# Kernel tuning notes

Hardware: AMD Instinct MI355X
Metric: run time of the kernel (lower is better)

Reference implementation:

```python
import jax, jax.numpy as jnp
import numpy as np

B, NR, IC, NC, OC = 64, 16384, 16, 10, 16
NUM_ITERS = 3


def setup_inputs() -> dict:
    key = jax.random.key(0)
    k1, k2, k3, k4 = jax.random.split(key, 4)
    x = jax.random.normal(k1, (B, NR, IC), dtype=jnp.float32)
    W = jax.random.normal(k2, (IC, NC, OC, NR), dtype=jnp.float32)
    fc_w = jax.random.normal(k3, (1, NC * OC), dtype=jnp.float32)
    fc_b = jax.random.normal(k4, (1,), dtype=jnp.float32)
    return {"x": x, "W": W, "fc_w": fc_w, "fc_b": fc_b}


def _squash(s):
    # Original squash is applied to tensors with trailing dim of size 1,
    # so the norm reduction is elementwise: s^2 * s / ((1+s^2) * sqrt(s^2))
    sq = s * s
    return sq * s / ((1.0 + sq) * jnp.sqrt(sq))


def reference(x, W, fc_w, fc_b):
    batch = x.shape[0]
    in_ch, nc, oc, nr = W.shape
    # u_hat[b,i,c,o] = sum_r W[i,c,o,r] * x[b,r,i]  (x is identical across capsules)
    u_hat = jnp.einsum('icor,bri->bico', W, x)  # [B, in_ch, nc, oc]
    b_ij = jnp.zeros((in_ch, nc), dtype=x.dtype)
    v_j = None
    for it in range(NUM_ITERS):
        c_ij = jax.nn.softmax(b_ij, axis=0)              # softmax over in_channels
        s_j = jnp.einsum('ic,bico->bco', c_ij, u_hat)    # [B, nc, oc]
        v_j = _squash(s_j)
        if it < NUM_ITERS - 1:
            # agreement a[b,i,c] = sum_o u_hat[b,i,c,o] * v[b,c,o]; mean over batch
            a_ij = jnp.einsum('bico,bco->ic', u_hat, v_j) / batch
            b_ij = b_ij + a_ij
    pred = jax.nn.sigmoid(v_j.reshape(batch, -1) @ fc_w.T + fc_b)[:, 0]  # [B]
    return pred, v_j[..., None]  # v_j returned as [B, nc, oc, 1] like torch
```

## Files before the change

### kernel.cpp

```cpp
#include <hip/hip_runtime.h>

typedef unsigned int uint;
typedef unsigned short ushort;
typedef __attribute__((ext_vector_type(8))) short bf16x8;
typedef __attribute__((ext_vector_type(4))) float floatx4;
typedef __attribute__((ext_vector_type(4))) uint uint4v;

#define B_   64
#define NR_  16384
#define IC_  16
#define NC_  10
#define OC_  16
#define NCO  160
#define KC_  32
#define KT_  32

__device__ __forceinline__ float bf2f(ushort h) {
    return __uint_as_float(((uint)h) << 16);
}
__device__ __forceinline__ ushort f2bf(float f) {
    uint u = __float_as_uint(f);
    u += 0x7fffu + ((u >> 16) & 1u);
    return (ushort)(u >> 16);
}
__device__ __forceinline__ void splitbf(float f, ushort& h, ushort& l) {
    h = f2bf(f);
    l = f2bf(f - bf2f(h));
}
__device__ __forceinline__ float squashf(float s) {
    return s * fabsf(s) / (1.0f + s * s);
}

__global__ __launch_bounds__(256) void k_xT(const float* __restrict__ xf,
                                            ushort* __restrict__ xTh,
                                            ushort* __restrict__ xTl)
{
    const int chunk = blockIdx.x, b = blockIdx.y, t = threadIdx.x;
    const int r0 = chunk * 1024;
#pragma unroll
    for (int j = 0; j < 4; ++j) {
        int r = r0 + t + 256 * j;
        const float* row = xf + ((size_t)b * NR_ + r) * IC_;
        float vals[16];
        *(float4*)&vals[0]  = *(const float4*)row;
        *(float4*)&vals[4]  = *(const float4*)(row + 4);
        *(float4*)&vals[8]  = *(const float4*)(row + 8);
        *(float4*)&vals[12] = *(const float4*)(row + 12);
#pragma unroll
        for (int i = 0; i < 16; ++i) {
            ushort h, l;
            splitbf(vals[i], h, l);
            size_t idx = ((size_t)(i * B_ + b)) * NR_ + r;
            xTh[idx] = h;
            xTl[idx] = l;
        }
    }
}

__global__ __launch_bounds__(512) void k_uhat(const float* __restrict__ xf,
                                              const float* __restrict__ wf,
                                              const ushort* __restrict__ xTh,
                                              const ushort* __restrict__ xTl,
                                              int has_xt,
                                              float* __restrict__ uh)
{
    const int i    = blockIdx.x;
    const int kc   = blockIdx.y;
    const int tid  = threadIdx.x;
    const int lane = tid & 63;
    const int w    = tid >> 6;
    const int quad = lane >> 4;
    const int m16  = lane & 15;
    const int bt   = w & 3;
    const int cg   = w >> 2;

    __shared__ ushort Xh[64 * 40], Xl[64 * 40];
    __shared__ ushort Wh[160 * 40], Wl[160 * 40];

    floatx4 acc[5];
#pragma unroll
    for (int t = 0; t < 5; ++t) acc[t] = (floatx4){0.f, 0.f, 0.f, 0.f};

    const int r0 = kc * (NR_ / KC_);

    for (int st = 0; st < (NR_ / KC_) / KT_; ++st) {
        const int rb = r0 + st * KT_;
        __syncthreads();
        if (has_xt) {
            int t8 = tid & 255, bb = t8 >> 2, part = t8 & 3;
            size_t src = (size_t)(i * B_ + bb) * NR_ + rb + part * 8;
            if (tid < 256)
                *(uint4v*)&Xh[bb * 40 + part * 8] = *(const uint4v*)&xTh[src];
            else
                *(uint4v*)&Xl[bb * 40 + part * 8] = *(const uint4v*)&xTl[src];
        } else {
#pragma unroll
            for (int s = 0; s < 4; ++s) {
                int n = tid + 512 * s;
                int bb = n >> 5, k = n & 31;
                float v = xf[(size_t)bb * (NR_ * IC_) + (size_t)(rb + k) * IC_ + i];
                ushort h, l;
                splitbf(v, h, l);
                Xh[bb * 40 + k] = h;
                Xl[bb * 40 + k] = l;
            }
        }
        for (int j = tid; j < 640; j += 512) {
            int row = j >> 2, seg = j & 3;
            const float* wp = wf + (size_t)(i * NCO + row) * NR_ + rb + seg * 8;
            float4 f0 = *(const float4*)wp;
            float4 f1 = *(const float4*)(wp + 4);
            float v[8] = {f0.x, f0.y, f0.z, f0.w, f1.x, f1.y, f1.z, f1.w};
            ushort hh[8], ll[8];
#pragma unroll
            for (int q = 0; q < 8; ++q) splitbf(v[q], hh[q], ll[q]);
            uint4v ph, pl;
#pragma unroll
            for (int q = 0; q < 4; ++q) {
                ph[q] = (uint)hh[2 * q] | ((uint)hh[2 * q + 1] << 16);
                pl[q] = (uint)ll[2 * q] | ((uint)ll[2 * q + 1] << 16);
            }
            *(uint4v*)&Wh[row * 40 + seg * 8] = ph;
            *(uint4v*)&Wl[row * 40 + seg * 8] = pl;
        }
        __syncthreads();
        bf16x8 afh = *(const bf16x8*)&Xh[(bt * 16 + m16) * 40 + quad * 8];
        bf16x8 afl = *(const bf16x8*)&Xl[(bt * 16 + m16) * 40 + quad * 8];
#pragma unroll
        for (int t = 0; t < 5; ++t) {
            int corow = (cg * 5 + t) * 16 + m16;
            bf16x8 bh = *(const bf16x8*)&Wh[corow * 40 + quad * 8];
            bf16x8 bl = *(const bf16x8*)&Wl[corow * 40 + quad * 8];
            acc[t] = __builtin_amdgcn_mfma_f32_16x16x32_bf16(afh, bh, acc[t], 0, 0, 0);
            acc[t] = __builtin_amdgcn_mfma_f32_16x16x32_bf16(afl, bh, acc[t], 0, 0, 0);
            acc[t] = __builtin_amdgcn_mfma_f32_16x16x32_bf16(afh, bl, acc[t], 0, 0, 0);
        }
    }
#pragma unroll
    for (int t = 0; t < 5; ++t) {
        int co = (cg * 5 + t) * 16 + m16;
#pragma unroll
        for (int r = 0; r < 4; ++r) {
            int b = bt * 16 + quad * 4 + r;
            atomicAdd(&uh[(b * IC_ + i) * NCO + co], acc[t][r]);
        }
    }
}

__global__ __launch_bounds__(256) void k_route1(const float* __restrict__ uh,
                                                float* __restrict__ a1)
{
    const int b = blockIdx.x, tid = threadIdx.x;
    __shared__ float vL[NCO];
    const float* ub = uh + b * IC_ * NCO;
    if (tid < NCO) {
        float s = 0.f;
#pragma unroll
        for (int i = 0; i < IC_; ++i) s += ub[i * NCO + tid];
        vL[tid] = squashf(s * (1.0f / 16.0f));
    }
    __syncthreads();
    if (tid < NCO) {
        int i = tid / NC_, c = tid - i * NC_;
        float sum = 0.f;
#pragma unroll
        for (int o = 0; o < OC_; ++o)
            sum += ub[i * NCO + c * OC_ + o] * vL[c * OC_ + o];
        atomicAdd(&a1[i * NC_ + c], sum * (1.0f / 64.0f));
    }
}

__global__ __launch_bounds__(256) void k_route2(const float* __restrict__ uh,
                                                const float* __restrict__ a1,
                                                float* __restrict__ a2)
{
    const int b = blockIdx.x, tid = threadIdx.x;
    __shared__ float aL[NCO];
    __shared__ float vL[NCO];
    if (tid < NCO) aL[tid] = a1[tid];
    __syncthreads();
    const float* ub = uh + b * IC_ * NCO;
    if (tid < NCO) {
        int c = tid >> 4;
        float m = -1e30f;
        for (int i = 0; i < IC_; ++i) m = fmaxf(m, aL[i * NC_ + c]);
        float Z = 0.f;
        for (int i = 0; i < IC_; ++i) Z += expf(aL[i * NC_ + c] - m);
        float s = 0.f;
        for (int i = 0; i < IC_; ++i)
            s += (expf(aL[i * NC_ + c] - m) / Z) * ub[i * NCO + tid];
        vL[tid] = squashf(s);
    }
    __syncthreads();
    if (tid < NCO) {
        int i = tid / NC_, c = tid - i * NC_;
        float sum = 0.f;
#pragma unroll
        for (int o = 0; o < OC_; ++o)
            sum += ub[i * NCO + c * OC_ + o] * vL[c * OC_ + o];
        atomicAdd(&a2[i * NC_ + c], sum * (1.0f / 64.0f));
    }
}

__global__ __launch_bounds__(256) void k_route3(const float* __restrict__ uh,
                                                const float* __restrict__ a1,
                                                const float* __restrict__ a2,
                                                const float* __restrict__ fcw,
                                                const float* __restrict__ fcb,
                                                float* __restrict__ out)
{
    const int b = blockIdx.x, tid = threadIdx.x;
    __shared__ float bL[NCO];
    __shared__ float pL[NCO];
    if (tid < NCO) bL[tid] = a1[tid] + a2[tid];
    __syncthreads();
    const float* ub = uh + b * IC_ * NCO;
    if (tid < NCO) {
        int c = tid >> 4;
        float m = -1e30f;
        for (int i = 0; i < IC_; ++i) m = fmaxf(m, bL[i * NC_ + c]);
        float Z = 0.f;
        for (int i = 0; i < IC_; ++i) Z += expf(bL[i * NC_ + c] - m);
        float s = 0.f;
        for (int i = 0; i < IC_; ++i)
            s += (expf(bL[i * NC_ + c] - m) / Z) * ub[i * NCO + tid];
        float v = squashf(s);
        out[64 + b * NCO + tid] = v;
        pL[tid] = v * fcw[tid];
    }
    __syncthreads();
    if (tid == 0) {
        float accv = fcb[0];
        for (int j = 0; j < NCO; ++j) accv += pL[j];
        out[b] = 1.0f / (1.0f + expf(-accv));
    }
}

extern "C" void kernel_launch(void* const* d_in, const int* in_sizes, int n_in,
                              void* d_out, int out_size, void* d_ws, size_t ws_size,
                              hipStream_t stream)
{
    const float* x   = (const float*)d_in[0];
    const float* W   = (const float*)d_in[1];
    const float* fcw = (const float*)d_in[2];
    const float* fcb = (const float*)d_in[3];
    float* out = (float*)d_out;

    float* uh = (float*)d_ws;
    float* a1 = uh + B_ * IC_ * NCO;
    float* a2 = a1 + NCO;
    const size_t xt_off   = 1u << 20;
    const size_t xt_bytes = (size_t)IC_ * B_ * NR_ * 2;
    ushort* xTh = (ushort*)((char*)d_ws + xt_off);
    ushort* xTl = (ushort*)((char*)d_ws + xt_off + xt_bytes);
    const int has_xt = (ws_size >= xt_off + 2 * xt_bytes) ? 1 : 0;

    hipMemsetAsync(d_ws, 0, (size_t)(B_ * IC_ * NCO + 2 * NCO) * sizeof(float), stream);
    if (has_xt)
        k_xT<<<dim3(16, 64), 256, 0, stream>>>(x, xTh, xTl);
    k_uhat<<<dim3(IC_, KC_), 512, 0, stream>>>(x, W, xTh, xTl, has_xt, uh);
    k_route1<<<B_, 256, 0, stream>>>(uh, a1);
    k_route2<<<B_, 256, 0, stream>>>(uh, a1, a2);
    k_route3<<<B_, 256, 0, stream>>>(uh, a1, a2, fcw, fcb, out);
}
```

Measured before the change: 321.8 us.

## Double-buffer W tiles in uhat GEMM and fuse routing into one kernel

```diff
diff --git a/kernel.cpp b/kernel.cpp
--- a/kernel.cpp
+++ b/kernel.cpp
@@ -4,7 +4,6 @@
 typedef unsigned short ushort;
 typedef __attribute__((ext_vector_type(8))) short bf16x8;
 typedef __attribute__((ext_vector_type(4))) float floatx4;
-typedef __attribute__((ext_vector_type(4))) uint uint4v;
 
 #define B_   64
 #define NR_  16384
@@ -14,6 +13,7 @@
 #define NCO  160
 #define KC_  32
 #define KT_  32
+#define NSTEP 16
 
 __device__ __forceinline__ float bf2f(ushort h) {
     return __uint_as_float(((uint)h) << 16);
@@ -33,9 +33,15 @@
 
 __global__ __launch_bounds__(256) void k_xT(const float* __restrict__ xf,
                                             ushort* __restrict__ xTh,
-                                            ushort* __restrict__ xTl)
+                                            ushort* __restrict__ xTl,
+                                            float* __restrict__ uh)
 {
     const int chunk = blockIdx.x, b = blockIdx.y, t = threadIdx.x;
+    if (chunk == 0) {
+        float4 z = {0.f, 0.f, 0.f, 0.f};
+        float4* dst = (float4*)(uh + (size_t)b * (IC_ * NCO));
+        for (int n = t; n < 640; n += 256) dst[n] = z;
+    }
     const int r0 = chunk * 1024;
 #pragma unroll
     for (int j = 0; j < 4; ++j) {
@@ -57,12 +63,80 @@
     }
 }
 
-__global__ __launch_bounds__(512) void k_uhat(const float* __restrict__ xf,
-                                              const float* __restrict__ wf,
-                                              const ushort* __restrict__ xTh,
-                                              const ushort* __restrict__ xTl,
-                                              int has_xt,
-                                              float* __restrict__ uh)
+__device__ __forceinline__ void loadW5(const float* __restrict__ wbase_st,
+                                       int tid, float2* r)
+{
+#pragma unroll
+    for (int s = 0; s < 5; ++s) {
+        int idx2 = tid + 512 * s;
+        int row  = idx2 >> 4;
+        int e    = idx2 & 15;
+        r[s] = *(const float2*)(wbase_st + (size_t)row * NR_ + 2 * e);
+    }
+}
+
+__device__ __forceinline__ void storeW5(const float2* r, int tid,
+                                        ushort* __restrict__ WhB,
+                                        ushort* __restrict__ WlB)
+{
+#pragma unroll
+    for (int s = 0; s < 5; ++s) {
+        int idx2 = tid + 512 * s;
+        int row  = idx2 >> 4;
+        int e    = idx2 & 15;
+        ushort h0, l0, h1, l1;
+        splitbf(r[s].x, h0, l0);
+        splitbf(r[s].y, h1, l1);
+        *(uint*)&WhB[row * 40 + 2 * e] = (uint)h0 | ((uint)h1 << 16);
+        *(uint*)&WlB[row * 40 + 2 * e] = (uint)l0 | ((uint)l1 << 16);
+    }
+}
+
+__device__ __forceinline__ void loadX(const ushort* __restrict__ xTh,
+                                      const ushort* __restrict__ xTl,
+                                      size_t xrow, int st, int has_xt,
+                                      const float* __restrict__ xf,
+                                      int b, int i, int r0, int quad,
+                                      bf16x8& h, bf16x8& l)
+{
+    if (has_xt) {
+        size_t o = xrow + (size_t)st * KT_;
+        h = *(const bf16x8*)&xTh[o];
+        l = *(const bf16x8*)&xTl[o];
+    } else {
+#pragma unroll
+        for (int q = 0; q < 8; ++q) {
+            float v = xf[((size_t)b * NR_ + r0 + st * KT_ + quad * 8 + q) * IC_ + i];
+            ushort hh, ll;
+            splitbf(v, hh, ll);
+            h[q] = (short)hh;
+            l[q] = (short)ll;
+        }
+    }
+}
+
+__device__ __forceinline__ void mfma5(const ushort* __restrict__ WhB,
+                                      const ushort* __restrict__ WlB,
+                                      bf16x8 ah, bf16x8 al,
+                                      floatx4* acc, int cg, int m16, int quad)
+{
+#pragma unroll
+    for (int t5 = 0; t5 < 5; ++t5) {
+        int corow = (cg * 5 + t5) * 16 + m16;
+        bf16x8 bh = *(const bf16x8*)&WhB[corow * 40 + quad * 8];
+        bf16x8 bl = *(const bf16x8*)&WlB[corow * 40 + quad * 8];
+        acc[t5] = __builtin_amdgcn_mfma_f32_16x16x32_bf16(ah, bh, acc[t5], 0, 0, 0);
+        acc[t5] = __builtin_amdgcn_mfma_f32_16x16x32_bf16(al, bh, acc[t5], 0, 0, 0);
+        acc[t5] = __builtin_amdgcn_mfma_f32_16x16x32_bf16(ah, bl, acc[t5], 0, 0, 0);
+    }
+}
+
+__global__ __launch_bounds__(512, 4) void k_uhat(const float* __restrict__ xf,
+                                                 const float* __restrict__ wf,
+                                                 const ushort* __restrict__ xTh,
+                                                 const ushort* __restrict__ xTl,
+                                                 int has_xt,
+                                                 float* __restrict__ uh)
 {
     const int i    = blockIdx.x;
     const int kc   = blockIdx.y;
@@ -74,165 +148,173 @@
     const int bt   = w & 3;
     const int cg   = w >> 2;
 
-    __shared__ ushort Xh[64 * 40], Xl[64 * 40];
-    __shared__ ushort Wh[160 * 40], Wl[160 * 40];
+    __shared__ ushort Wh[2][160 * 40];
+    __shared__ ushort Wl[2][160 * 40];
 
     floatx4 acc[5];
 #pragma unroll
     for (int t = 0; t < 5; ++t) acc[t] = (floatx4){0.f, 0.f, 0.f, 0.f};
 
     const int r0 = kc * (NR_ / KC_);
-
-    for (int st = 0; st < (NR_ / KC_) / KT_; ++st) {
-        const int rb = r0 + st * KT_;
+    const float* wbase = wf + (size_t)i * NCO * NR_ + r0;
+    const int xb = bt * 16 + m16;
+    const size_t xrow = (size_t)(i * B_ + xb) * NR_ + r0 + quad * 8;
+
+    float2 wA[5], wB[5];
+    bf16x8 xhA, xlA, xhB, xlB;
+
+    loadW5(wbase, tid, wA);
+    loadX(xTh, xTl, xrow, 0, has_xt, xf, xb, i, r0, quad, xhA, xlA);
+    storeW5(wA, tid, Wh[0], Wl[0]);
+    loadW5(wbase + 1 * KT_, tid, wB);
+    __syncthreads();
+
+    for (int st = 0; st < NSTEP; st += 2) {
+        loadX(xTh, xTl, xrow, st + 1, has_xt, xf, xb, i, r0, quad, xhB, xlB);
+        storeW5(wB, tid, Wh[1], Wl[1]);
+        if (st + 2 < NSTEP) loadW5(wbase + (size_t)(st + 2) * KT_, tid, wA);
+        mfma5(Wh[0], Wl[0], xhA, xlA, acc, cg, m16, quad);
         __syncthreads();
-        if (has_xt) {
-            int t8 = tid & 255, bb = t8 >> 2, part = t8 & 3;
-            size_t src = (size_t)(i * B_ + bb) * NR_ + rb + part * 8;
-            if (tid < 256)
-                *(uint4v*)&Xh[bb * 40 + part * 8] = *(const uint4v*)&xTh[src];
-            else
-                *(uint4v*)&Xl[bb * 40 + part * 8] = *(const uint4v*)&xTl[src];
-        } else {
-#pragma unroll
-            for (int s = 0; s < 4; ++s) {
-                int n = tid + 512 * s;
-                int bb = n >> 5, k = n & 31;
-                float v = xf[(size_t)bb * (NR_ * IC_) + (size_t)(rb + k) * IC_ + i];
-                ushort h, l;
-                splitbf(v, h, l);
-                Xh[bb * 40 + k] = h;
-                Xl[bb * 40 + k] = l;
-            }
-        }
-        for (int j = tid; j < 640; j += 512) {
-            int row = j >> 2, seg = j & 3;
-            const float* wp = wf + (size_t)(i * NCO + row) * NR_ + rb + seg * 8;
-            float4 f0 = *(const float4*)wp;
-            float4 f1 = *(const float4*)(wp + 4);
-            float v[8] = {f0.x, f0.y, f0.z, f0.w, f1.x, f1.y, f1.z, f1.w};
-            ushort hh[8], ll[8];
-#pragma unroll
-            for (int q = 0; q < 8; ++q) splitbf(v[q], hh[q], ll[q]);
-            uint4v ph, pl;
-#pragma unroll
-            for (int q = 0; q < 4; ++q) {
-                ph[q] = (uint)hh[2 * q] | ((uint)hh[2 * q + 1] << 16);
-                pl[q] = (uint)ll[2 * q] | ((uint)ll[2 * q + 1] << 16);
-            }
-            *(uint4v*)&Wh[row * 40 + seg * 8] = ph;
-            *(uint4v*)&Wl[row * 40 + seg * 8] = pl;
-        }
+
+        if (st + 2 < NSTEP) {
+            loadX(xTh, xTl, xrow, st + 2, has_xt, xf, xb, i, r0, quad, xhA, xlA);
+            storeW5(wA, tid, Wh[0], Wl[0]);
+        }
+        if (st + 3 < NSTEP) loadW5(wbase + (size_t)(st + 3) * KT_, tid, wB);
+        mfma5(Wh[1], Wl[1], xhB, xlB, acc, cg, m16, quad);
         __syncthreads();
-        bf16x8 afh = *(const bf16x8*)&Xh[(bt * 16 + m16) * 40 + quad * 8];
-        bf16x8 afl = *(const bf16x8*)&Xl[(bt * 16 + m16) * 40 + quad * 8];
-#pragma unroll
-        for (int t = 0; t < 5; ++t) {
-            int corow = (cg * 5 + t) * 16 + m16;
-            bf16x8 bh = *(const bf16x8*)&Wh[corow * 40 + quad * 8];
-            bf16x8 bl = *(const bf16x8*)&Wl[corow * 40 + quad * 8];
-            acc[t] = __builtin_amdgcn_mfma_f32_16x16x32_bf16(afh, bh, acc[t], 0, 0, 0);
-            acc[t] = __builtin_amdgcn_mfma_f32_16x16x32_bf16(afl, bh, acc[t], 0, 0, 0);
-            acc[t] = __builtin_amdgcn_mfma_f32_16x16x32_bf16(afh, bl, acc[t], 0, 0, 0);
-        }
-    }
-#pragma unroll
-    for (int t = 0; t < 5; ++t) {
-        int co = (cg * 5 + t) * 16 + m16;
+    }
+
+#pragma unroll
+    for (int t5 = 0; t5 < 5; ++t5) {
+        int co = (cg * 5 + t5) * 16 + m16;
 #pragma unroll
         for (int r = 0; r < 4; ++r) {
             int b = bt * 16 + quad * 4 + r;
-            atomicAdd(&uh[(b * IC_ + i) * NCO + co], acc[t][r]);
-        }
-    }
-}
-
-__global__ __launch_bounds__(256) void k_route1(const float* __restrict__ uh,
-                                                float* __restrict__ a1)
-{
-    const int b = blockIdx.x, tid = threadIdx.x;
-    __shared__ float vL[NCO];
-    const float* ub = uh + b * IC_ * NCO;
-    if (tid < NCO) {
+            atomicAdd(&uh[(b * IC_ + i) * NCO + co], acc[t5][r]);
+        }
+    }
+}
+
+__global__ __launch_bounds__(256) void k_route(const float* __restrict__ uh,
+                                               const float* __restrict__ fcw,
+                                               const float* __restrict__ fcb,
+                                               float* __restrict__ out)
+{
+    const int bo = blockIdx.x, t = threadIdx.x;
+    __shared__ float vL[B_ * NCO];
+    __shared__ float a1L[160];
+    __shared__ float bL[160];
+    __shared__ float cL[160];
+
+    for (int q4 = t; q4 < 2560; q4 += 256) {
+        int b = q4 / 40, r = q4 - b * 40;
+        const float4* up = (const float4*)(uh + (size_t)b * 2560 + r * 4);
+        float4 s = {0.f, 0.f, 0.f, 0.f};
+#pragma unroll
+        for (int i2 = 0; i2 < 16; ++i2) {
+            float4 u4 = up[i2 * 40];
+            s.x += u4.x; s.y += u4.y; s.z += u4.z; s.w += u4.w;
+        }
+        float4 v;
+        v.x = squashf(s.x * 0.0625f);
+        v.y = squashf(s.y * 0.0625f);
+        v.z = squashf(s.z * 0.0625f);
+        v.w = squashf(s.w * 0.0625f);
+        *((float4*)vL + q4) = v;
+    }
+    __syncthreads();
+    if (t < 160) {
+        int c = t >> 4, i2 = t & 15;
+        const float* up0 = uh + i2 * NCO + c * 16;
+        const float* vp0 = vL + c * 16;
+        float4 s4 = {0.f, 0.f, 0.f, 0.f};
+        for (int b = 0; b < 64; ++b) {
+            const float4* up = (const float4*)(up0 + (size_t)b * 2560);
+            const float4* vp = (const float4*)(vp0 + b * 160);
+#pragma unroll
+            for (int q = 0; q < 4; ++q) {
+                float4 u4 = up[q], v4 = vp[q];
+                s4.x += u4.x * v4.x; s4.y += u4.y * v4.y;
+                s4.z += u4.z * v4.z; s4.w += u4.w * v4.w;
+            }
+        }
+        a1L[t] = ((s4.x + s4.y) + (s4.z + s4.w)) * (1.0f / 64.0f);
+    }
+    __syncthreads();
+    if (t < 160) {
+        int c = t >> 4;
+        float m = -1e30f;
+#pragma unroll
+        for (int i2 = 0; i2 < 16; ++i2) m = fmaxf(m, a1L[c * 16 + i2]);
+        float Z = 0.f;
+#pragma unroll
+        for (int i2 = 0; i2 < 16; ++i2) Z += expf(a1L[c * 16 + i2] - m);
+        cL[t] = expf(a1L[t] - m) / Z;
+    }
+    __syncthreads();
+    for (int q4 = t; q4 < 2560; q4 += 256) {
+        int b = q4 / 40, r = q4 - b * 40;
+        int c = r >> 2;
+        const float4* up = (const float4*)(uh + (size_t)b * 2560 + r * 4);
+        float4 s = {0.f, 0.f, 0.f, 0.f};
+#pragma unroll
+        for (int i2 = 0; i2 < 16; ++i2) {
+            float w2 = cL[c * 16 + i2];
+            float4 u4 = up[i2 * 40];
+            s.x += w2 * u4.x; s.y += w2 * u4.y;
+            s.z += w2 * u4.z; s.w += w2 * u4.w;
+        }
+        float4 v;
+        v.x = squashf(s.x); v.y = squashf(s.y);
+        v.z = squashf(s.z); v.w = squashf(s.w);
+        *((float4*)vL + q4) = v;
+    }
+    __syncthreads();
+    if (t < 160) {
+        int c = t >> 4, i2 = t & 15;
+        const float* up0 = uh + i2 * NCO + c * 16;
+        const float* vp0 = vL + c * 16;
+        float4 s4 = {0.f, 0.f, 0.f, 0.f};
+        for (int b = 0; b < 64; ++b) {
+            const float4* up = (const float4*)(up0 + (size_t)b * 2560);
+            const float4* vp = (const float4*)(vp0 + b * 160);
+#pragma unroll
+            for (int q = 0; q < 4; ++q) {
+                float4 u4 = up[q], v4 = vp[q];
+                s4.x += u4.x * v4.x; s4.y += u4.y * v4.y;
+                s4.z += u4.z * v4.z; s4.w += u4.w * v4.w;
+            }
+        }
+        bL[t] = a1L[t] + ((s4.x + s4.y) + (s4.z + s4.w)) * (1.0f / 64.0f);
+    }
+    __syncthreads();
+    if (t < 160) {
+        int c = t >> 4;
+        float m = -1e30f;
+#pragma unroll
+        for (int i2 = 0; i2 < 16; ++i2) m = fmaxf(m, bL[c * 16 + i2]);
+        float Z = 0.f;
+#pragma unroll
+        for (int i2 = 0; i2 < 16; ++i2) Z += expf(bL[c * 16 + i2] - m);
+        cL[t] = expf(bL[t] - m) / Z;
+    }
+    __syncthreads();
+    if (t < 160) {
+        int c = t >> 4;
+        const float* ub = uh + (size_t)bo * 2560 + t;
         float s = 0.f;
 #pragma unroll
-        for (int i = 0; i < IC_; ++i) s += ub[i * NCO + tid];
-        vL[tid] = squashf(s * (1.0f / 16.0f));
-    }
-    __syncthreads();
-    if (tid < NCO) {
-        int i = tid / NC_, c = tid - i * NC_;
-        float sum = 0.f;
-#pragma unroll
-        for (int o = 0; o < OC_; ++o)
-            sum += ub[i * NCO + c * OC_ + o] * vL[c * OC_ + o];
-        atomicAdd(&a1[i * NC_ + c], sum * (1.0f / 64.0f));
-    }
-}
-
-__global__ __launch_bounds__(256) void k_route2(const float* __restrict__ uh,
-                                                const float* __restrict__ a1,
-                                                float* __restrict__ a2)
-{
-    const int b = blockIdx.x, tid = threadIdx.x;
-    __shared__ float aL[NCO];
-    __shared__ float vL[NCO];
-    if (tid < NCO) aL[tid] = a1[tid];
-    __syncthreads();
-    const float* ub = uh + b * IC_ * NCO;
-    if (tid < NCO) {
-        int c = tid >> 4;
-        float m = -1e30f;
-        for (int i = 0; i < IC_; ++i) m = fmaxf(m, aL[i * NC_ + c]);
-        float Z = 0.f;
-        for (int i = 0; i < IC_; ++i) Z += expf(aL[i * NC_ + c] - m);
-        float s = 0.f;
-        for (int i = 0; i < IC_; ++i)
-            s += (expf(aL[i * NC_ + c] - m) / Z) * ub[i * NCO + tid];
-        vL[tid] = squashf(s);
-    }
-    __syncthreads();
-    if (tid < NCO) {
-        int i = tid / NC_, c = tid - i * NC_;
-        float sum = 0.f;
-#pragma unroll
-        for (int o = 0; o < OC_; ++o)
-            sum += ub[i * NCO + c * OC_ + o] * vL[c * OC_ + o];
-        atomicAdd(&a2[i * NC_ + c], sum * (1.0f / 64.0f));
-    }
-}
-
-__global__ __launch_bounds__(256) void k_route3(const float* __restrict__ uh,
-                                                const float* __restrict__ a1,
-                                                const float* __restrict__ a2,
-                                                const float* __restrict__ fcw,
-                                                const float* __restrict__ fcb,
-                                                float* __restrict__ out)
-{
-    const int b = blockIdx.x, tid = threadIdx.x;
-    __shared__ float bL[NCO];
-    __shared__ float pL[NCO];
-    if (tid < NCO) bL[tid] = a1[tid] + a2[tid];
-    __syncthreads();
-    const float* ub = uh + b * IC_ * NCO;
-    if (tid < NCO) {
-        int c = tid >> 4;
-        float m = -1e30f;
-        for (int i = 0; i < IC_; ++i) m = fmaxf(m, bL[i * NC_ + c]);
-        float Z = 0.f;
-        for (int i = 0; i < IC_; ++i) Z += expf(bL[i * NC_ + c] - m);
-        float s = 0.f;
-        for (int i = 0; i < IC_; ++i)
-            s += (expf(bL[i * NC_ + c] - m) / Z) * ub[i * NCO + tid];
+        for (int i2 = 0; i2 < 16; ++i2) s += cL[c * 16 + i2] * ub[i2 * NCO];
         float v = squashf(s);
-        out[64 + b * NCO + tid] = v;
-        pL[tid] = v * fcw[tid];
-    }
-    __syncthreads();
-    if (tid == 0) {
-        float accv = fcb[0];
-        for (int j = 0; j < NCO; ++j) accv += pL[j];
-        out[b] = 1.0f / (1.0f + expf(-accv));
+        out[64 + bo * NCO + t] = v;
+        bL[t] = v * fcw[t];
+    }
+    __syncthreads();
+    if (t == 0) {
+        float a = fcb[0];
+        for (int j = 0; j < 160; ++j) a += bL[j];
+        out[bo] = 1.0f / (1.0f + expf(-a));
     }
 }
 
@@ -247,19 +329,17 @@
     float* out = (float*)d_out;
 
     float* uh = (float*)d_ws;
-    float* a1 = uh + B_ * IC_ * NCO;
-    float* a2 = a1 + NCO;
     const size_t xt_off   = 1u << 20;
     const size_t xt_bytes = (size_t)IC_ * B_ * NR_ * 2;
     ushort* xTh = (ushort*)((char*)d_ws + xt_off);
     ushort* xTl = (ushort*)((char*)d_ws + xt_off + xt_bytes);
     const int has_xt = (ws_size >= xt_off + 2 * xt_bytes) ? 1 : 0;
 
-    hipMemsetAsync(d_ws, 0, (size_t)(B_ * IC_ * NCO + 2 * NCO) * sizeof(float), stream);
-    if (has_xt)
-        k_xT<<<dim3(16, 64), 256, 0, stream>>>(x, xTh, xTl);
+    if (has_xt) {
+        k_xT<<<dim3(16, 64), 256, 0, stream>>>(x, xTh, xTl, uh);
+    } else {
+        hipMemsetAsync(uh, 0, (size_t)(B_ * IC_ * NCO) * sizeof(float), stream);
+    }
     k_uhat<<<dim3(IC_, KC_), 512, 0, stream>>>(x, W, xTh, xTl, has_xt, uh);
-    k_route1<<<B_, 256, 0, stream>>>(uh, a1);
-    k_route2<<<B_, 256, 0, stream>>>(uh, a1, a2);
-    k_route3<<<B_, 256, 0, stream>>>(uh, a1, a2, fcw, fcb, out);
-}
+    k_route<<<B_, 256, 0, stream>>>(uh, fcw, fcb, out);
+}
```

After: 355.7 us. +10.5%, slower.

## Fuse routing kernels into one cooperative kernel and fold memset into transpose

Applied to the files above, without the earlier changes.

```diff
diff --git a/kernel.cpp b/kernel.cpp
--- a/kernel.cpp
+++ b/kernel.cpp
@@ -1,4 +1,7 @@
 #include <hip/hip_runtime.h>
+#include <hip/hip_cooperative_groups.h>
+
+namespace cg = cooperative_groups;
 
 typedef unsigned int uint;
 typedef unsigned short ushort;
@@ -33,9 +36,19 @@
 
 __global__ __launch_bounds__(256) void k_xT(const float* __restrict__ xf,
                                             ushort* __restrict__ xTh,
-                                            ushort* __restrict__ xTl)
+                                            ushort* __restrict__ xTl,
+                                            float* __restrict__ uh)
 {
     const int chunk = blockIdx.x, b = blockIdx.y, t = threadIdx.x;
+    if (chunk == 0) {
+        float4 z = {0.f, 0.f, 0.f, 0.f};
+        float4* dst = (float4*)(uh + (size_t)b * (IC_ * NCO));
+        for (int n = t; n < 640; n += 256) dst[n] = z;
+        if (b == 0 && t < 80) {
+            float4* da = (float4*)(uh + (size_t)B_ * IC_ * NCO);
+            da[t] = z;
+        }
+    }
     const int r0 = chunk * 1024;
 #pragma unroll
     for (int j = 0; j < 4; ++j) {
@@ -72,7 +85,7 @@
     const int quad = lane >> 4;
     const int m16  = lane & 15;
     const int bt   = w & 3;
-    const int cg   = w >> 2;
+    const int cg_  = w >> 2;
 
     __shared__ ushort Xh[64 * 40], Xl[64 * 40];
     __shared__ ushort Wh[160 * 40], Wl[160 * 40];
@@ -127,32 +140,39 @@
         bf16x8 afh = *(const bf16x8*)&Xh[(bt * 16 + m16) * 40 + quad * 8];
         bf16x8 afl = *(const bf16x8*)&Xl[(bt * 16 + m16) * 40 + quad * 8];
 #pragma unroll
-        for (int t = 0; t < 5; ++t) {
-            int corow = (cg * 5 + t) * 16 + m16;
+        for (int t5 = 0; t5 < 5; ++t5) {
+            int corow = (cg_ * 5 + t5) * 16 + m16;
             bf16x8 bh = *(const bf16x8*)&Wh[corow * 40 + quad * 8];
             bf16x8 bl = *(const bf16x8*)&Wl[corow * 40 + quad * 8];
-            acc[t] = __builtin_amdgcn_mfma_f32_16x16x32_bf16(afh, bh, acc[t], 0, 0, 0);
-            acc[t] = __builtin_amdgcn_mfma_f32_16x16x32_bf16(afl, bh, acc[t], 0, 0, 0);
-            acc[t] = __builtin_amdgcn_mfma_f32_16x16x32_bf16(afh, bl, acc[t], 0, 0, 0);
-        }
-    }
-#pragma unroll
-    for (int t = 0; t < 5; ++t) {
-        int co = (cg * 5 + t) * 16 + m16;
+            acc[t5] = __builtin_amdgcn_mfma_f32_16x16x32_bf16(afh, bh, acc[t5], 0, 0, 0);
+            acc[t5] = __builtin_amdgcn_mfma_f32_16x16x32_bf16(afl, bh, acc[t5], 0, 0, 0);
+            acc[t5] = __builtin_amdgcn_mfma_f32_16x16x32_bf16(afh, bl, acc[t5], 0, 0, 0);
+        }
+    }
+#pragma unroll
+    for (int t5 = 0; t5 < 5; ++t5) {
+        int co = (cg_ * 5 + t5) * 16 + m16;
 #pragma unroll
         for (int r = 0; r < 4; ++r) {
             int b = bt * 16 + quad * 4 + r;
-            atomicAdd(&uh[(b * IC_ + i) * NCO + co], acc[t][r]);
-        }
-    }
-}
-
-__global__ __launch_bounds__(256) void k_route1(const float* __restrict__ uh,
-                                                float* __restrict__ a1)
-{
+            atomicAdd(&uh[(b * IC_ + i) * NCO + co], acc[t5][r]);
+        }
+    }
+}
+
+__global__ __launch_bounds__(256) void k_route_coop(const float* __restrict__ uh,
+                                                    float* __restrict__ a1,
+                                                    float* __restrict__ a2,
+                                                    const float* __restrict__ fcw,
+                                                    const float* __restrict__ fcb,
+                                                    float* __restrict__ out)
+{
+    cg::grid_group grid = cg::this_grid();
     const int b = blockIdx.x, tid = threadIdx.x;
     __shared__ float vL[NCO];
+    __shared__ float aL[NCO];
     const float* ub = uh + b * IC_ * NCO;
+
     if (tid < NCO) {
         float s = 0.f;
 #pragma unroll
@@ -168,23 +188,18 @@
             sum += ub[i * NCO + c * OC_ + o] * vL[c * OC_ + o];
         atomicAdd(&a1[i * NC_ + c], sum * (1.0f / 64.0f));
     }
-}
-
-__global__ __launch_bounds__(256) void k_route2(const float* __restrict__ uh,
-                                                const float* __restrict__ a1,
-                                                float* __restrict__ a2)
-{
-    const int b = blockIdx.x, tid = threadIdx.x;
-    __shared__ float aL[NCO];
-    __shared__ float vL[NCO];
+    __threadfence();
+    grid.sync();
+
     if (tid < NCO) aL[tid] = a1[tid];
     __syncthreads();
-    const float* ub = uh + b * IC_ * NCO;
     if (tid < NCO) {
         int c = tid >> 4;
         float m = -1e30f;
+#pragma unroll
         for (int i = 0; i < IC_; ++i) m = fmaxf(m, aL[i * NC_ + c]);
         float Z = 0.f;
+#pragma unroll
         for (int i = 0; i < IC_; ++i) Z += expf(aL[i * NC_ + c] - m);
         float s = 0.f;
         for (int i = 0; i < IC_; ++i)
@@ -200,39 +215,31 @@
             sum += ub[i * NCO + c * OC_ + o] * vL[c * OC_ + o];
         atomicAdd(&a2[i * NC_ + c], sum * (1.0f / 64.0f));
     }
-}
-
-__global__ __launch_bounds__(256) void k_route3(const float* __restrict__ uh,
-                                                const float* __restrict__ a1,
-                                                const float* __restrict__ a2,
-                                                const float* __restrict__ fcw,
-                                                const float* __restrict__ fcb,
-                                                float* __restrict__ out)
-{
-    const int b = blockIdx.x, tid = threadIdx.x;
-    __shared__ float bL[NCO];
-    __shared__ float pL[NCO];
-    if (tid < NCO) bL[tid] = a1[tid] + a2[tid];
-    __syncthreads();
-    const float* ub = uh + b * IC_ * NCO;
+    __threadfence();
+    grid.sync();
+
+    if (tid < NCO) aL[tid] = a1[tid] + a2[tid];
+    __syncthreads();
     if (tid < NCO) {
         int c = tid >> 4;
         float m = -1e30f;
-        for (int i = 0; i < IC_; ++i) m = fmaxf(m, bL[i * NC_ + c]);
+#pragma unroll
+        for (int i = 0; i < IC_; ++i) m = fmaxf(m, aL[i * NC_ + c]);
         float Z = 0.f;
-        for (int i = 0; i < IC_; ++i) Z += expf(bL[i * NC_ + c] - m);
+#pragma unroll
+        for (int i = 0; i < IC_; ++i) Z += expf(aL[i * NC_ + c] - m);
         float s = 0.f;
         for (int i = 0; i < IC_; ++i)
-            s += (expf(bL[i * NC_ + c] - m) / Z) * ub[i * NCO + tid];
+            s += (expf(aL[i * NC_ + c] - m) / Z) * ub[i * NCO + tid];
         float v = squashf(s);
         out[64 + b * NCO + tid] = v;
-        pL[tid] = v * fcw[tid];
+        vL[tid] = v * fcw[tid];
     }
     __syncthreads();
     if (tid == 0) {
-        float accv = fcb[0];
-        for (int j = 0; j < NCO; ++j) accv += pL[j];
-        out[b] = 1.0f / (1.0f + expf(-accv));
+        float a = fcb[0];
+        for (int j = 0; j < NCO; ++j) a += vL[j];
+        out[b] = 1.0f / (1.0f + expf(-a));
     }
 }
 
@@ -255,11 +262,14 @@
     ushort* xTl = (ushort*)((char*)d_ws + xt_off + xt_bytes);
     const int has_xt = (ws_size >= xt_off + 2 * xt_bytes) ? 1 : 0;
 
-    hipMemsetAsync(d_ws, 0, (size_t)(B_ * IC_ * NCO + 2 * NCO) * sizeof(float), stream);
-    if (has_xt)
-        k_xT<<<dim3(16, 64), 256, 0, stream>>>(x, xTh, xTl);
+    if (has_xt) {
+        k_xT<<<dim3(16, 64), 256, 0, stream>>>(x, xTh, xTl, uh);
+    } else {
+        hipMemsetAsync(d_ws, 0, (size_t)(B_ * IC_ * NCO + 2 * NCO) * sizeof(float), stream);
+    }
     k_uhat<<<dim3(IC_, KC_), 512, 0, stream>>>(x, W, xTh, xTl, has_xt, uh);
-    k_route1<<<B_, 256, 0, stream>>>(uh, a1);
-    k_route2<<<B_, 256, 0, stream>>>(uh, a1, a2);
-    k_route3<<<B_, 256, 0, stream>>>(uh, a1, a2, fcw, fcb, out);
-}
+
+    void* args[] = {(void*)&uh, (void*)&a1, (void*)&a2,
+                    (void*)&fcw, (void*)&fcb, (void*)&out};
+    hipLaunchCooperativeKernel((void*)k_route_coop, dim3(B_), dim3(256), args, 0, stream);
+}
```

Result: slower. 360.1 us (+11.9%).
